# Kernel optimization log

Measured on AMD Instinct MI355X. Metric: run time of the kernel, lower is better.

## Reference

```python
import jax, jax.numpy as jnp
import numpy as np

B, S, D = 2, 2048, 4096
H, KVH, HD = 32, 8, 128
THETA = 10000.0


def setup_inputs() -> dict:
    key = jax.random.key(0)
    k1, k2, k3 = jax.random.split(key, 3)
    hidden_states = jax.random.normal(k1, (B, S, D), jnp.float32)
    w_qkv = jax.random.normal(k2, ((KVH * 2 + H) * HD, D), jnp.float32) * 0.02
    w_dense = jax.random.normal(k3, (D, D), jnp.float32) * 0.02
    return {"hidden_states": hidden_states, "w_qkv": w_qkv, "w_dense": w_dense}


def _rope(x, pos):
    # x: [B, H, S, HD]; Falcon rotary embedding (rotate_half convention)
    inv_freq = 1.0 / (THETA ** (jnp.arange(0, HD, 2, dtype=jnp.float32) / HD))
    freqs = pos[:, None] * inv_freq[None, :]           # [S, HD/2]
    emb = jnp.concatenate([freqs, freqs], axis=-1)      # [S, HD]
    cos, sin = jnp.cos(emb), jnp.sin(emb)
    x1, x2 = x[..., : HD // 2], x[..., HD // 2 :]
    rot = jnp.concatenate([-x2, x1], axis=-1)
    return x * cos + rot * sin


def reference(hidden_states, w_qkv, w_dense):
    # fused QKV projection (FalconLinear, no bias)
    fused = jnp.einsum('bsd,ed->bse', hidden_states, w_qkv)  # [B,S,(2KVH+H)*HD]
    g = H // KVH  # query heads per kv head
    qkv = fused.reshape(B, S, KVH, g + 2, HD)
    q = qkv[:, :, :, :g]                        # [B,S,KVH,g,HD]
    k = jnp.broadcast_to(qkv[:, :, :, g:g + 1], q.shape)
    v = jnp.broadcast_to(qkv[:, :, :, g + 1:g + 2], q.shape)
    q, k, v = (t.reshape(B, S, H, HD).transpose(0, 2, 1, 3) for t in (q, k, v))
    pos = jnp.arange(S, dtype=jnp.float32)
    q = _rope(q, pos)
    k = _rope(k, pos)
    scores = jnp.einsum('bhqd,bhkd->bhqk', q, k) / jnp.sqrt(jnp.float32(HD))
    causal = jnp.tril(jnp.ones((S, S), dtype=bool))
    scores = jnp.where(causal, scores, jnp.float32(-1e9))
    attn = jax.nn.softmax(scores, axis=-1)
    out = jnp.einsum('bhqk,bhkd->bhqd', attn, v)
    out = out.transpose(0, 2, 1, 3).reshape(B, S, H * HD)   # merge heads
    return jnp.einsum('bsd,ed->bse', out, w_dense)
```

## Files before the change

### kernel.cpp

```cpp
#include <hip/hip_runtime.h>

#define B_   2
#define S_   2048
#define D_   4096
#define H_   32
#define KVH_ 8
#define HD_  128
#define NE_  6144

using f32x4  = __attribute__((ext_vector_type(4))) float;
using bf16x8 = __attribute__((ext_vector_type(8))) __bf16;

__device__ __forceinline__ unsigned short f2bf(float f) {
  union { float f; unsigned u; } v; v.f = f;
  unsigned r = v.u + 0x7FFFu + ((v.u >> 16) & 1u);
  return (unsigned short)(r >> 16);
}
__device__ __forceinline__ float bf2f(unsigned short h) {
  union { unsigned u; float f; } v; v.u = ((unsigned)h) << 16; return v.f;
}
__device__ __forceinline__ bf16x8 ld8(const unsigned short* p) {
  return *reinterpret_cast<const bf16x8*>(p);
}
__device__ __forceinline__ bf16x8 ld8b(const void* base, int byte_off) {
  return *reinterpret_cast<const bf16x8*>((const char*)base + byte_off);
}
__device__ __forceinline__ void cp16(const void* g, void* l) {
  __builtin_amdgcn_global_load_lds(
      (const __attribute__((address_space(1))) void*)g,
      (__attribute__((address_space(3))) void*)l, 16, 0, 0);
}
__device__ __forceinline__ float exp2a(float x) {
  float r; asm("v_exp_f32 %0, %1" : "=v"(r) : "v"(x)); return r;
}

__global__ __launch_bounds__(256) void cvt_f32_bf16(
    const float* __restrict__ in, unsigned short* __restrict__ out, int n4)
{
  int i = blockIdx.x * 256 + threadIdx.x;
  if (i >= n4) return;
  f32x4 v = *reinterpret_cast<const f32x4*>(in + (size_t)i * 4);
  ushort4 o;
  o.x = f2bf(v[0]); o.y = f2bf(v[1]); o.z = f2bf(v[2]); o.w = f2bf(v[3]);
  *reinterpret_cast<ushort4*>(out + (size_t)i * 4) = o;
}

__global__ __launch_bounds__(256) void cvt2_f32_bf16(
    const float* __restrict__ s0, unsigned short* __restrict__ d0, int n0,
    const float* __restrict__ s1, unsigned short* __restrict__ d1, int n1)
{
  int i = blockIdx.x * 256 + threadIdx.x;
  const float* src; unsigned short* dst;
  if (i < n0) { src = s0; dst = d0; }
  else        { i -= n0; if (i >= n1) return; src = s1; dst = d1; }
  f32x4 v = *reinterpret_cast<const f32x4*>(src + (size_t)i * 4);
  ushort4 o;
  o.x = f2bf(v[0]); o.y = f2bf(v[1]); o.z = f2bf(v[2]); o.w = f2bf(v[3]);
  *reinterpret_cast<ushort4*>(dst + (size_t)i * 4) = o;
}

template <typename OutT, int NT>
__global__ __launch_bounds__(512, 2) void gemm256(
    const unsigned short* __restrict__ A,
    const unsigned short* __restrict__ Bw,
    OutT* __restrict__ C, int M, int N)
{
  constexpr int K  = 4096;
  constexpr int NI = (K / 64) / 2;
  constexpr int NB = NT / 64;
  constexpr int NN = NT / 64;
  constexpr int WN = NT / 4;
  constexpr int BBUF = NT * 128;
  __shared__ __align__(16) char lds[65536 + 2 * BBUF];

  const int tid  = threadIdx.x;
  const int lane = tid & 63;
  const int wave = tid >> 6;
  const int wr = wave >> 2;
  const int wc = wave & 3;
  const int lr = lane & 15;
  const int lk = (lane >> 4) * 8;

  int id  = blockIdx.y * gridDim.x + blockIdx.x;
  const int nwg = gridDim.x * gridDim.y;
  if ((nwg & 7) == 0) { const int q = nwg >> 3; id = (id & 7) * q + (id >> 3); }
  const int row0 = (id / gridDim.x) * 256;
  const int col0 = (id % gridDim.x) * NT;

  int rwA[2], csA[2], dbA[2];
#pragma unroll
  for (int j = 0; j < 2; ++j) {
    dbA[j] = j * 8192 + tid * 16;
    rwA[j] = dbA[j] >> 7;
    csA[j] = ((dbA[j] & 127) ^ ((rwA[j] & 7) << 4)) >> 1;
  }
  auto stA = [&](int buf, int h, int t) {
#pragma unroll
    for (int j = 0; j < 2; ++j)
      cp16(A + (size_t)(row0 + h * 128 + rwA[j]) * K + t * 64 + csA[j],
           lds + buf * 32768 + h * 16384 + dbA[j]);
  };
  const int dbB = tid * 16;
  const int rwB = dbB >> 7;
  const int csB = ((dbB & 127) ^ ((rwB & 7) << 4)) >> 1;
  auto stB = [&](int buf, int c, int t) {
    cp16(Bw + (size_t)(col0 + c * 64 + rwB) * K + t * 64 + csB,
         lds + 65536 + buf * BBUF + c * 8192 + dbB);
  };

  const int cb0 = ((0 + lk) << 1) ^ ((lr & 7) << 4);
  const int cb1 = ((32 + lk) << 1) ^ ((lr & 7) << 4);
  const int aRowB = (wr * 128 + lr) * 128;
  const int bRowB = (wc * WN + lr) * 128;

  f32x4 acc[8][NN];
#pragma unroll
  for (int m = 0; m < 8; ++m)
#pragma unroll
    for (int n = 0; n < NN; ++n) acc[m][n] = (f32x4){0.f, 0.f, 0.f, 0.f};
  bf16x8 bfr[NN][2];

#define FENCE asm volatile("" ::: "memory")
#define VMNB  do { if constexpr (NB == 4) asm volatile("s_waitcnt vmcnt(4)" ::: "memory"); \
                   else                   asm volatile("s_waitcnt vmcnt(3)" ::: "memory"); } while (0)
#define VM0   asm volatile("s_waitcnt vmcnt(0)" ::: "memory")

#define PHASE(p, buf, STAGE, WAIT)                                             \
  {                                                                            \
    if ((p) == 0) {                                                            \
      _Pragma("unroll")                                                        \
      for (int n = 0; n < NN; ++n) {                                           \
        bfr[n][0] = ld8b(lds, 65536 + (buf) * BBUF + bRowB + n * 2048 + cb0);  \
        bfr[n][1] = ld8b(lds, 65536 + (buf) * BBUF + bRowB + n * 2048 + cb1);  \
      }                                                                        \
    }                                                                          \
    bf16x8 a00 = ld8b(lds, (buf) * 32768 + aRowB + ((p) * 2 + 0) * 2048 + cb0);\
    bf16x8 a01 = ld8b(lds, (buf) * 32768 + aRowB + ((p) * 2 + 0) * 2048 + cb1);\
    bf16x8 a10 = ld8b(lds, (buf) * 32768 + aRowB + ((p) * 2 + 1) * 2048 + cb0);\
    bf16x8 a11 = ld8b(lds, (buf) * 32768 + aRowB + ((p) * 2 + 1) * 2048 + cb1);\
    STAGE;                                                                     \
    FENCE;                                                                     \
    __builtin_amdgcn_s_barrier();                                              \
    __builtin_amdgcn_s_setprio(1);                                             \
    _Pragma("unroll")                                                          \
    for (int n = 0; n < NN; ++n) {                                             \
      acc[(p)*2+0][n] = __builtin_amdgcn_mfma_f32_16x16x32_bf16(a00, bfr[n][0], acc[(p)*2+0][n], 0, 0, 0); \
      acc[(p)*2+0][n] = __builtin_amdgcn_mfma_f32_16x16x32_bf16(a01, bfr[n][1], acc[(p)*2+0][n], 0, 0, 0); \
      acc[(p)*2+1][n] = __builtin_amdgcn_mfma_f32_16x16x32_bf16(a10, bfr[n][0], acc[(p)*2+1][n], 0, 0, 0); \
      acc[(p)*2+1][n] = __builtin_amdgcn_mfma_f32_16x16x32_bf16(a11, bfr[n][1], acc[(p)*2+1][n], 0, 0, 0); \
    }                                                                          \
    __builtin_amdgcn_s_setprio(0);                                             \
    WAIT;                                                                      \
    FENCE;                                                                     \
    __builtin_amdgcn_s_barrier();                                              \
  }

#pragma unroll
  for (int c = 0; c < NB; ++c) stB(0, c, 0);
  stA(0, 0, 0); stA(0, 1, 0);
#pragma unroll
  for (int c = 0; c < NB; ++c) stB(1, c, 1);
  VMNB;
  FENCE;
  __builtin_amdgcn_s_barrier();

  for (int i = 0; i < NI; ++i) {
    const int t1  = 2 * i + 1;
    const int tn0 = 2 * i + 2;
    const int tn1 = 2 * i + 3;
    const bool pre = (i + 1 < NI);
    PHASE(0, 0, { stA(1, 0, t1); }, {});
    PHASE(1, 0, { stA(1, 1, t1); }, {});
    PHASE(2, 0, { if (pre) { stB(0, 0, tn0); stB(0, 1, tn0); } }, {});
    PHASE(3, 0, { if (pre) { _Pragma("unroll") for (int c = 2; c < NB; ++c) stB(0, c, tn0); } },
          { if (pre) { VMNB; } else { VM0; } });
    PHASE(0, 1, { if (pre) stA(0, 0, tn0); }, {});
    PHASE(1, 1, { if (pre) stA(0, 1, tn0); }, {});
    PHASE(2, 1, { if (pre) { stB(1, 0, tn1); stB(1, 1, tn1); } }, {});
    PHASE(3, 1, { if (pre) { _Pragma("unroll") for (int c = 2; c < NB; ++c) stB(1, c, tn1); } },
          { if (pre) { VMNB; } });
  }
#undef PHASE
#undef FENCE
#undef VMNB
#undef VM0

  const int orow = (lane >> 4) * 4;
#pragma unroll
  for (int m = 0; m < 8; ++m) {
    const int gr0 = row0 + wr * 128 + m * 16 + orow;
#pragma unroll
    for (int n = 0; n < NN; ++n) {
      const int gc = col0 + wc * WN + n * 16 + lr;
#pragma unroll
      for (int r = 0; r < 4; ++r) {
        float val = acc[m][n][r];
        if constexpr (sizeof(OutT) == 2)
          C[(size_t)(gr0 + r) * N + gc] = f2bf(val);
        else
          C[(size_t)(gr0 + r) * N + gc] = val;
      }
    }
  }
}

__global__ __launch_bounds__(256) void rope_scatter(
    const unsigned short* __restrict__ fused,
    unsigned short* __restrict__ Qr,
    unsigned short* __restrict__ Kr,
    unsigned short* __restrict__ Vt)
{
  int idx = blockIdx.x * 256 + threadIdx.x;
  int d = idx & 63;
  int t = idx >> 6;
  int e = t % 48;
  int bs = t / 48;
  int s = bs % S_;
  int b = bs / S_;
  int kvh = e / 6, j = e % 6;
  const unsigned short* src = fused + (size_t)bs * NE_ + e * 128;
  unsigned short u1 = src[d];
  unsigned short u2 = src[d + 64];
  if (j == 5) {
    size_t base = (size_t)(b * KVH_ + kvh) * HD_ * S_;
    Vt[base + (size_t)d * S_ + s]        = u1;
    Vt[base + (size_t)(d + 64) * S_ + s] = u2;
  } else {
    float x1 = bf2f(u1), x2 = bf2f(u2);
    float inv = __expf(-(float)d * (9.2103403719761836f / 64.0f));
    float ang = (float)s * inv;
    float sn, c;
    sincosf(ang, &sn, &c);
    float o1 = x1 * c - x2 * sn;
    float o2 = x2 * c + x1 * sn;
    unsigned short* dst;
    if (j == 4) dst = Kr + ((size_t)(b * KVH_ + kvh) * S_ + s) * HD_;
    else        dst = Qr + ((size_t)(b * H_ + kvh * 4 + j) * S_ + s) * HD_;
    dst[d]      = f2bf(o1);
    dst[d + 64] = f2bf(o2);
  }
}

__global__ __launch_bounds__(256) void attn_fwd(
    const unsigned short* __restrict__ Qr,
    const unsigned short* __restrict__ Kr,
    const unsigned short* __restrict__ Vt,
    unsigned short* __restrict__ O)
{
  __shared__ __align__(16) unsigned short Kld[2][64 * 128];
  __shared__ __align__(16) unsigned short Vld[2][128 * 64];
  __shared__ __align__(16) unsigned short Pld[4][16 * 64];

  const int tid  = threadIdx.x;
  const int lane = tid & 63;
  const int wave = tid >> 6;
  const int bx = blockIdx.x;
  const int h  = blockIdx.y;
  const int b  = blockIdx.z;
  const int kvh = h >> 2;
  const int lr = lane & 15;
  const int lk = (lane >> 4) * 8;
  const int orow = (lane >> 4) * 4;

  const float SC2 = 0.08838834764831845f * 1.4426950408889634f;
  const unsigned short* Kb = Kr + (size_t)(b * KVH_ + kvh) * S_ * HD_;
  const unsigned short* Vb = Vt + (size_t)(b * KVH_ + kvh) * HD_ * S_;

  auto stage = [&](int buf, int kb) {
#pragma unroll
    for (int i = 0; i < 4; ++i) {
      const int db = i * 4096 + tid * 16;
      {
        const int row  = db >> 8;
        const int colb = (db & 255) ^ ((row & 7) << 4);
        cp16(Kb + (size_t)(kb * 64 + row) * HD_ + (colb >> 1),
             (char*)&Kld[buf][0] + i * 4096 + wave * 1024);
      }
      {
        const int row  = db >> 7;
        const int colb = (db & 127) ^ ((row & 7) << 4);
        cp16(Vb + (size_t)row * S_ + kb * 64 + (colb >> 1),
             (char*)&Vld[buf][0] + i * 4096 + wave * 1024);
      }
    }
  };

  for (int half = 0; half < 2; ++half) {
    const int qb = half ? (S_ / 64 - 1 - bx) : bx;

    const unsigned short* qbase =
        Qr + ((size_t)(b * H_ + h) * S_ + qb * 64 + wave * 16 + lr) * HD_;
    bf16x8 qf[4];
#pragma unroll
    for (int t = 0; t < 4; ++t) {
      union { bf16x8 v; unsigned short s[8]; } u;
      u.v = ld8(qbase + t * 32 + lk);
#pragma unroll
      for (int j = 0; j < 8; ++j) u.s[j] = f2bf(bf2f(u.s[j]) * SC2);
      qf[t] = u.v;
    }

    f32x4 acc_o[8];
#pragma unroll
    for (int dt = 0; dt < 8; ++dt) acc_o[dt] = (f32x4){0.f, 0.f, 0.f, 0.f};
    float mrow[4], lpart[4];
#pragma unroll
    for (int r = 0; r < 4; ++r) { mrow[r] = -1e30f; lpart[r] = 0.f; }

    stage(0, 0);
    __syncthreads();

    for (int kb = 0; kb <= qb; ++kb) {
      const int cur = kb & 1;
      if (kb < qb) stage(cur ^ 1, kb + 1);

      const char* Kc = (const char*)&Kld[cur][0];
      const char* Vc = (const char*)&Vld[cur][0];

      f32x4 accs[4];
#pragma unroll
      for (int kt = 0; kt < 4; ++kt) accs[kt] = (f32x4){0.f, 0.f, 0.f, 0.f};
      __builtin_amdgcn_s_setprio(1);
#pragma unroll
      for (int t = 0; t < 4; ++t) {
#pragma unroll
        for (int kt = 0; kt < 4; ++kt) {
          const int krow = kt * 16 + lr;
          const int kbyte = ((krow << 8) + ((t * 32 + lk) << 1)) ^ ((krow & 7) << 4);
          bf16x8 kf = ld8b(Kc, kbyte);
          accs[kt] = __builtin_amdgcn_mfma_f32_16x16x32_bf16(qf[t], kf, accs[kt], 0, 0, 0);
        }
      }
      __builtin_amdgcn_s_setprio(0);

      if (kb == qb) {
#pragma unroll
        for (int r = 0; r < 4; ++r) {
          const int qg = wave * 16 + orow + r;
#pragma unroll
          for (int kt = 0; kt < 4; ++kt)
            if (kt * 16 + lr > qg) accs[kt][r] = -1e30f;
        }
      }

      float mx[4];
#pragma unroll
      for (int r = 0; r < 4; ++r)
        mx[r] = fmaxf(fmaxf(accs[0][r], accs[1][r]), fmaxf(accs[2][r], accs[3][r]));
      int ok = (mx[0] <= mrow[0] + 8.f) && (mx[1] <= mrow[1] + 8.f) &&
               (mx[2] <= mrow[2] + 8.f) && (mx[3] <= mrow[3] + 8.f);
      if (!__all(ok)) {
        float corr[4];
#pragma unroll
        for (int r = 0; r < 4; ++r) {
          float m = mx[r];
#pragma unroll
          for (int msk = 8; msk >= 1; msk >>= 1) m = fmaxf(m, __shfl_xor(m, msk, 64));
          float mnew = fmaxf(mrow[r], m);
          corr[r] = exp2a(mrow[r] - mnew);
          mrow[r] = mnew;
          lpart[r] *= corr[r];
        }
#pragma unroll
        for (int dt = 0; dt < 8; ++dt)
#pragma unroll
          for (int r = 0; r < 4; ++r) acc_o[dt][r] *= corr[r];
      }

#pragma unroll
      for (int r = 0; r < 4; ++r) {
        const int prow = orow + r;
#pragma unroll
        for (int kt = 0; kt < 4; ++kt) {
          float p = exp2a(accs[kt][r] - mrow[r]);
          lpart[r] += p;
          const int pbyte = ((prow << 7) + ((kt * 16 + lr) << 1)) ^ ((prow & 7) << 4);
          *(__bf16*)((char*)&Pld[wave][0] + pbyte) = (__bf16)p;
        }
      }

      asm volatile("" ::: "memory");

      __builtin_amdgcn_s_setprio(1);
#pragma unroll
      for (int kc = 0; kc < 2; ++kc) {
        const int pbyte = ((lr << 7) + ((kc * 32 + lk) << 1)) ^ ((lr & 7) << 4);
        bf16x8 pf = ld8b(&Pld[wave][0], pbyte);
#pragma unroll
        for (int dt = 0; dt < 8; ++dt) {
          const int vrow = dt * 16 + lr;
          const int vbyte = ((vrow << 7) + ((kc * 32 + lk) << 1)) ^ ((vrow & 7) << 4);
          bf16x8 vf = ld8b(Vc, vbyte);
          acc_o[dt] = __builtin_amdgcn_mfma_f32_16x16x32_bf16(pf, vf, acc_o[dt], 0, 0, 0);
        }
      }
      __builtin_amdgcn_s_setprio(0);

      __syncthreads();
    }

#pragma unroll
    for (int r = 0; r < 4; ++r) {
      float s = lpart[r];
#pragma unroll
      for (int msk = 8; msk >= 1; msk >>= 1) s += __shfl_xor(s, msk, 64);
      float inv = 1.f / s;
      size_t rowoff =
          (size_t)(b * S_ + qb * 64 + wave * 16 + orow + r) * (H_ * HD_) + h * HD_;
#pragma unroll
      for (int dt = 0; dt < 8; ++dt)
        O[rowoff + dt * 16 + lr] = f2bf(acc_o[dt][r] * inv);
    }
  }
}

__global__ void fill_sentinel(float* __restrict__ O, int n) {
  int i = blockIdx.x * 256 + threadIdx.x;
  if (i < n) O[i] = 12345.0f;
}

extern "C" void kernel_launch(void* const* d_in, const int* in_sizes, int n_in,
                              void* d_out, int out_size, void* d_ws, size_t ws_size,
                              hipStream_t stream) {
  const float* hidden = (const float*)d_in[0];
  const float* wqkv   = (const float*)d_in[1];
  const float* wdense = (const float*)d_in[2];
  float* out = (float*)d_out;

  const size_t NEED = 134217728;
  if (ws_size < NEED) {
    fill_sentinel<<<dim3((out_size + 255) / 256), dim3(256), 0, stream>>>(out, out_size);
    return;
  }

  char* ws = (char*)d_ws;
  unsigned short* Hb    = (unsigned short*)(ws);
  unsigned short* Wqb   = (unsigned short*)(ws + 33554432);
  unsigned short* fused = (unsigned short*)(ws + 83886080);
  unsigned short* Qr    = (unsigned short*)(ws);
  unsigned short* Kr    = (unsigned short*)(ws + 33554432);
  unsigned short* Vt    = (unsigned short*)(ws + 41943040);
  unsigned short* Wdb   = (unsigned short*)(ws + 50331648);
  unsigned short* attn_out = (unsigned short*)(ws + 83886080);

  const int nH4 = B_ * S_ * D_ / 4;
  const int nQ4 = NE_ * D_ / 4;
  const int nD4 = D_ * D_ / 4;

  cvt2_f32_bf16<<<dim3((nH4 + nQ4 + 255) / 256), dim3(256), 0, stream>>>(
      hidden, Hb, nH4, wqkv, Wqb, nQ4);

  gemm256<unsigned short, 192><<<dim3(NE_ / 192, (B_ * S_) / 256), dim3(512), 0, stream>>>(
      Hb, Wqb, fused, B_ * S_, NE_);

  cvt_f32_bf16<<<dim3(nD4 / 256), dim3(256), 0, stream>>>(wdense, Wdb, nD4);

  rope_scatter<<<dim3((B_ * S_ * 48 * 64) / 256), dim3(256), 0, stream>>>(
      fused, Qr, Kr, Vt);

  attn_fwd<<<dim3(16, H_, B_), dim3(256), 0, stream>>>(Qr, Kr, Vt, attn_out);

  gemm256<float, 256><<<dim3(D_ / 256, (B_ * S_) / 256), dim3(512), 0, stream>>>(
      attn_out, Wdb, out, B_ * S_, D_);
}
```

Before: 527.4 us.

## Double attention query tile per wave to reuse K/V loads and vectorize rope scatter

The attention kernel now processes 128 query rows per block (32 per wave, two 16-row fragments) instead of 64. Each K and V fragment read from shared memory feeds two MFMAs, and the number of K/V tile loads per query drops. The grid shrinks to 8 blocks per head pair-half, which means fewer blocks and more register pressure. Separately, rope_scatter now handles 8 elements per thread with 16-byte vector loads and stores for Q/K, while V is still written element by element with strided stores.

```diff
diff --git a/kernel.cpp b/kernel.cpp
--- a/kernel.cpp
+++ b/kernel.cpp
@@ -10,6 +10,7 @@
 
 using f32x4  = __attribute__((ext_vector_type(4))) float;
 using bf16x8 = __attribute__((ext_vector_type(8))) __bf16;
+using u16x8  = __attribute__((ext_vector_type(8))) unsigned short;
 
 __device__ __forceinline__ unsigned short f2bf(float f) {
   union { float f; unsigned u; } v; v.f = f;
@@ -211,33 +212,41 @@
     unsigned short* __restrict__ Vt)
 {
   int idx = blockIdx.x * 256 + threadIdx.x;
-  int d = idx & 63;
-  int t = idx >> 6;
+  int dg = idx & 7;
+  int t = idx >> 3;
   int e = t % 48;
   int bs = t / 48;
   int s = bs % S_;
   int b = bs / S_;
   int kvh = e / 6, j = e % 6;
-  const unsigned short* src = fused + (size_t)bs * NE_ + e * 128;
-  unsigned short u1 = src[d];
-  unsigned short u2 = src[d + 64];
+  const unsigned short* src = fused + (size_t)bs * NE_ + e * 128 + dg * 8;
+  u16x8 lo = *reinterpret_cast<const u16x8*>(src);
+  u16x8 hi = *reinterpret_cast<const u16x8*>(src + 64);
   if (j == 5) {
-    size_t base = (size_t)(b * KVH_ + kvh) * HD_ * S_;
-    Vt[base + (size_t)d * S_ + s]        = u1;
-    Vt[base + (size_t)(d + 64) * S_ + s] = u2;
+    size_t base = (size_t)(b * KVH_ + kvh) * HD_ * S_ + s;
+#pragma unroll
+    for (int jj = 0; jj < 8; ++jj) {
+      Vt[base + (size_t)(dg * 8 + jj) * S_]      = lo[jj];
+      Vt[base + (size_t)(dg * 8 + jj + 64) * S_] = hi[jj];
+    }
   } else {
-    float x1 = bf2f(u1), x2 = bf2f(u2);
-    float inv = __expf(-(float)d * (9.2103403719761836f / 64.0f));
-    float ang = (float)s * inv;
-    float sn, c;
-    sincosf(ang, &sn, &c);
-    float o1 = x1 * c - x2 * sn;
-    float o2 = x2 * c + x1 * sn;
+    u16x8 olo, ohi;
+#pragma unroll
+    for (int jj = 0; jj < 8; ++jj) {
+      int d = dg * 8 + jj;
+      float x1 = bf2f(lo[jj]), x2 = bf2f(hi[jj]);
+      float inv = __expf(-(float)d * (9.2103403719761836f / 64.0f));
+      float ang = (float)s * inv;
+      float sn, c;
+      sincosf(ang, &sn, &c);
+      olo[jj] = f2bf(x1 * c - x2 * sn);
+      ohi[jj] = f2bf(x2 * c + x1 * sn);
+    }
     unsigned short* dst;
     if (j == 4) dst = Kr + ((size_t)(b * KVH_ + kvh) * S_ + s) * HD_;
     else        dst = Qr + ((size_t)(b * H_ + kvh * 4 + j) * S_ + s) * HD_;
-    dst[d]      = f2bf(o1);
-    dst[d + 64] = f2bf(o2);
+    *reinterpret_cast<u16x8*>(dst + dg * 8)      = olo;
+    *reinterpret_cast<u16x8*>(dst + dg * 8 + 64) = ohi;
   }
 }
 
@@ -249,7 +258,7 @@
 {
   __shared__ __align__(16) unsigned short Kld[2][64 * 128];
   __shared__ __align__(16) unsigned short Vld[2][128 * 64];
-  __shared__ __align__(16) unsigned short Pld[4][16 * 64];
+  __shared__ __align__(16) unsigned short Pld[4][32 * 64];
 
   const int tid  = threadIdx.x;
   const int lane = tid & 63;
@@ -286,40 +295,50 @@
   };
 
   for (int half = 0; half < 2; ++half) {
-    const int qb = half ? (S_ / 64 - 1 - bx) : bx;
-
-    const unsigned short* qbase =
-        Qr + ((size_t)(b * H_ + h) * S_ + qb * 64 + wave * 16 + lr) * HD_;
-    bf16x8 qf[4];
-#pragma unroll
-    for (int t = 0; t < 4; ++t) {
-      union { bf16x8 v; unsigned short s[8]; } u;
-      u.v = ld8(qbase + t * 32 + lk);
-#pragma unroll
-      for (int j = 0; j < 8; ++j) u.s[j] = f2bf(bf2f(u.s[j]) * SC2);
-      qf[t] = u.v;
+    const int qt = half ? (15 - bx) : bx;
+    const int nkb = 2 * (qt + 1);
+
+    bf16x8 qf[2][4];
+#pragma unroll
+    for (int fr = 0; fr < 2; ++fr) {
+      const unsigned short* qbase =
+          Qr + ((size_t)(b * H_ + h) * S_ + qt * 128 + wave * 32 + fr * 16 + lr) * HD_;
+#pragma unroll
+      for (int t = 0; t < 4; ++t) {
+        union { bf16x8 v; unsigned short s2[8]; } u;
+        u.v = ld8(qbase + t * 32 + lk);
+#pragma unroll
+        for (int jj = 0; jj < 8; ++jj) u.s2[jj] = f2bf(bf2f(u.s2[jj]) * SC2);
+        qf[fr][t] = u.v;
+      }
     }
 
-    f32x4 acc_o[8];
-#pragma unroll
-    for (int dt = 0; dt < 8; ++dt) acc_o[dt] = (f32x4){0.f, 0.f, 0.f, 0.f};
-    float mrow[4], lpart[4];
-#pragma unroll
-    for (int r = 0; r < 4; ++r) { mrow[r] = -1e30f; lpart[r] = 0.f; }
+    f32x4 acc_o[2][8];
+#pragma unroll
+    for (int fr = 0; fr < 2; ++fr)
+#pragma unroll
+      for (int dt = 0; dt < 8; ++dt) acc_o[fr][dt] = (f32x4){0.f, 0.f, 0.f, 0.f};
+    float mrow[2][4], lpart[2][4];
+#pragma unroll
+    for (int fr = 0; fr < 2; ++fr)
+#pragma unroll
+      for (int r = 0; r < 4; ++r) { mrow[fr][r] = -1e30f; lpart[fr][r] = 0.f; }
 
     stage(0, 0);
     __syncthreads();
 
-    for (int kb = 0; kb <= qb; ++kb) {
+    for (int kb = 0; kb < nkb; ++kb) {
       const int cur = kb & 1;
-      if (kb < qb) stage(cur ^ 1, kb + 1);
+      if (kb + 1 < nkb) stage(cur ^ 1, kb + 1);
 
       const char* Kc = (const char*)&Kld[cur][0];
       const char* Vc = (const char*)&Vld[cur][0];
 
-      f32x4 accs[4];
-#pragma unroll
-      for (int kt = 0; kt < 4; ++kt) accs[kt] = (f32x4){0.f, 0.f, 0.f, 0.f};
+      f32x4 accs[2][4];
+#pragma unroll
+      for (int fr = 0; fr < 2; ++fr)
+#pragma unroll
+        for (int kt = 0; kt < 4; ++kt) accs[fr][kt] = (f32x4){0.f, 0.f, 0.f, 0.f};
       __builtin_amdgcn_s_setprio(1);
 #pragma unroll
       for (int t = 0; t < 4; ++t) {
@@ -328,70 +347,91 @@
           const int krow = kt * 16 + lr;
           const int kbyte = ((krow << 8) + ((t * 32 + lk) << 1)) ^ ((krow & 7) << 4);
           bf16x8 kf = ld8b(Kc, kbyte);
-          accs[kt] = __builtin_amdgcn_mfma_f32_16x16x32_bf16(qf[t], kf, accs[kt], 0, 0, 0);
+          accs[0][kt] = __builtin_amdgcn_mfma_f32_16x16x32_bf16(qf[0][t], kf, accs[0][kt], 0, 0, 0);
+          accs[1][kt] = __builtin_amdgcn_mfma_f32_16x16x32_bf16(qf[1][t], kf, accs[1][kt], 0, 0, 0);
         }
       }
       __builtin_amdgcn_s_setprio(0);
 
-      if (kb == qb) {
+      if (kb >= 2 * qt) {
+        const int koff = (kb - 2 * qt) * 64;
+#pragma unroll
+        for (int fr = 0; fr < 2; ++fr)
+#pragma unroll
+          for (int r = 0; r < 4; ++r) {
+            const int qg = wave * 32 + fr * 16 + orow + r;
+#pragma unroll
+            for (int kt = 0; kt < 4; ++kt)
+              if (koff + kt * 16 + lr > qg) accs[fr][kt][r] = -1e30f;
+          }
+      }
+
+      float mx[2][4];
+#pragma unroll
+      for (int fr = 0; fr < 2; ++fr)
+#pragma unroll
+        for (int r = 0; r < 4; ++r)
+          mx[fr][r] = fmaxf(fmaxf(accs[fr][0][r], accs[fr][1][r]),
+                            fmaxf(accs[fr][2][r], accs[fr][3][r]));
+      int ok = 1;
+#pragma unroll
+      for (int fr = 0; fr < 2; ++fr)
+#pragma unroll
+        for (int r = 0; r < 4; ++r) ok &= (mx[fr][r] <= mrow[fr][r] + 8.f);
+      if (!__all(ok)) {
+#pragma unroll
+        for (int fr = 0; fr < 2; ++fr) {
+          float corr[4];
+#pragma unroll
+          for (int r = 0; r < 4; ++r) {
+            float m = mx[fr][r];
+#pragma unroll
+            for (int msk = 8; msk >= 1; msk >>= 1) m = fmaxf(m, __shfl_xor(m, msk, 64));
+            float mnew = fmaxf(mrow[fr][r], m);
+            corr[r] = exp2a(mrow[fr][r] - mnew);
+            mrow[fr][r] = mnew;
+            lpart[fr][r] *= corr[r];
+          }
+#pragma unroll
+          for (int dt = 0; dt < 8; ++dt)
+#pragma unroll
+            for (int r = 0; r < 4; ++r) acc_o[fr][dt][r] *= corr[r];
+        }
+      }
+
+#pragma unroll
+      for (int fr = 0; fr < 2; ++fr)
 #pragma unroll
         for (int r = 0; r < 4; ++r) {
-          const int qg = wave * 16 + orow + r;
-#pragma unroll
-          for (int kt = 0; kt < 4; ++kt)
-            if (kt * 16 + lr > qg) accs[kt][r] = -1e30f;
+          const int prow = fr * 16 + orow + r;
+#pragma unroll
+          for (int kt = 0; kt < 4; ++kt) {
+            float p = exp2a(accs[fr][kt][r] - mrow[fr][r]);
+            lpart[fr][r] += p;
+            const int pbyte = ((prow << 7) + ((kt * 16 + lr) << 1)) ^ ((prow & 7) << 4);
+            *(__bf16*)((char*)&Pld[wave][0] + pbyte) = (__bf16)p;
+          }
         }
-      }
-
-      float mx[4];
-#pragma unroll
-      for (int r = 0; r < 4; ++r)
-        mx[r] = fmaxf(fmaxf(accs[0][r], accs[1][r]), fmaxf(accs[2][r], accs[3][r]));
-      int ok = (mx[0] <= mrow[0] + 8.f) && (mx[1] <= mrow[1] + 8.f) &&
-               (mx[2] <= mrow[2] + 8.f) && (mx[3] <= mrow[3] + 8.f);
-      if (!__all(ok)) {
-        float corr[4];
-#pragma unroll
-        for (int r = 0; r < 4; ++r) {
-          float m = mx[r];
-#pragma unroll
-          for (int msk = 8; msk >= 1; msk >>= 1) m = fmaxf(m, __shfl_xor(m, msk, 64));
-          float mnew = fmaxf(mrow[r], m);
-          corr[r] = exp2a(mrow[r] - mnew);
-          mrow[r] = mnew;
-          lpart[r] *= corr[r];
+
+      asm volatile("" ::: "memory");
+
+      __builtin_amdgcn_s_setprio(1);
+#pragma unroll
+      for (int kc = 0; kc < 2; ++kc) {
+        bf16x8 pf[2];
+#pragma unroll
+        for (int fr = 0; fr < 2; ++fr) {
+          const int pr = fr * 16 + lr;
+          pf[fr] = ld8b(&Pld[wave][0],
+                        ((pr << 7) + ((kc * 32 + lk) << 1)) ^ ((pr & 7) << 4));
         }
-#pragma unroll
-        for (int dt = 0; dt < 8; ++dt)
-#pragma unroll
-          for (int r = 0; r < 4; ++r) acc_o[dt][r] *= corr[r];
-      }
-
-#pragma unroll
-      for (int r = 0; r < 4; ++r) {
-        const int prow = orow + r;
-#pragma unroll
-        for (int kt = 0; kt < 4; ++kt) {
-          float p = exp2a(accs[kt][r] - mrow[r]);
-          lpart[r] += p;
-          const int pbyte = ((prow << 7) + ((kt * 16 + lr) << 1)) ^ ((prow & 7) << 4);
-          *(__bf16*)((char*)&Pld[wave][0] + pbyte) = (__bf16)p;
-        }
-      }
-
-      asm volatile("" ::: "memory");
-
-      __builtin_amdgcn_s_setprio(1);
-#pragma unroll
-      for (int kc = 0; kc < 2; ++kc) {
-        const int pbyte = ((lr << 7) + ((kc * 32 + lk) << 1)) ^ ((lr & 7) << 4);
-        bf16x8 pf = ld8b(&Pld[wave][0], pbyte);
 #pragma unroll
         for (int dt = 0; dt < 8; ++dt) {
           const int vrow = dt * 16 + lr;
           const int vbyte = ((vrow << 7) + ((kc * 32 + lk) << 1)) ^ ((vrow & 7) << 4);
           bf16x8 vf = ld8b(Vc, vbyte);
-          acc_o[dt] = __builtin_amdgcn_mfma_f32_16x16x32_bf16(pf, vf, acc_o[dt], 0, 0, 0);
+          acc_o[0][dt] = __builtin_amdgcn_mfma_f32_16x16x32_bf16(pf[0], vf, acc_o[0][dt], 0, 0, 0);
+          acc_o[1][dt] = __builtin_amdgcn_mfma_f32_16x16x32_bf16(pf[1], vf, acc_o[1][dt], 0, 0, 0);
         }
       }
       __builtin_amdgcn_s_setprio(0);
@@ -400,17 +440,19 @@
     }
 
 #pragma unroll
-    for (int r = 0; r < 4; ++r) {
-      float s = lpart[r];
-#pragma unroll
-      for (int msk = 8; msk >= 1; msk >>= 1) s += __shfl_xor(s, msk, 64);
-      float inv = 1.f / s;
-      size_t rowoff =
-          (size_t)(b * S_ + qb * 64 + wave * 16 + orow + r) * (H_ * HD_) + h * HD_;
-#pragma unroll
-      for (int dt = 0; dt < 8; ++dt)
-        O[rowoff + dt * 16 + lr] = f2bf(acc_o[dt][r] * inv);
-    }
+    for (int fr = 0; fr < 2; ++fr)
+#pragma unroll
+      for (int r = 0; r < 4; ++r) {
+        float s = lpart[fr][r];
+#pragma unroll
+        for (int msk = 8; msk >= 1; msk >>= 1) s += __shfl_xor(s, msk, 64);
+        float inv = 1.f / s;
+        size_t rowoff =
+            (size_t)(b * S_ + qt * 128 + wave * 32 + fr * 16 + orow + r) * (H_ * HD_) + h * HD_;
+#pragma unroll
+        for (int dt = 0; dt < 8; ++dt)
+          O[rowoff + dt * 16 + lr] = f2bf(acc_o[fr][dt][r] * inv);
+      }
   }
 }
 
@@ -455,10 +497,10 @@
 
   cvt_f32_bf16<<<dim3(nD4 / 256), dim3(256), 0, stream>>>(wdense, Wdb, nD4);
 
-  rope_scatter<<<dim3((B_ * S_ * 48 * 64) / 256), dim3(256), 0, stream>>>(
+  rope_scatter<<<dim3((B_ * S_ * 48 * 8) / 256), dim3(256), 0, stream>>>(
       fused, Qr, Kr, Vt);
 
-  attn_fwd<<<dim3(16, H_, B_), dim3(256), 0, stream>>>(Qr, Kr, Vt, attn_out);
+  attn_fwd<<<dim3(8, H_, B_), dim3(256), 0, stream>>>(Qr, Kr, Vt, attn_out);
 
   gemm256<float, 256><<<dim3(D_ / 256, (B_ * S_) / 256), dim3(512), 0, stream>>>(
       attn_out, Wdb, out, B_ * S_, D_);
```

Result: slower. 542.7 us (+2.9%).
